# Optimization experiments

Hardware: AMD Instinct MI355X
Metric: run time of the kernel (lower is better)

The kernel has to match this reference:

```python
import jax, jax.numpy as jnp
import numpy as np

N_QUBITS = 8
N_LAYERS = 1
DIM = 1 << N_QUBITS  # 256 statevector amplitudes; PennyLane wire 0 = most significant bit

_idx = np.arange(DIM)
_BITS = np.stack([(_idx >> (N_QUBITS - 1 - w)) & 1 for w in range(N_QUBITS)])  # (n, D)
_FLIP = np.stack([_idx ^ (1 << (N_QUBITS - 1 - w)) for w in range(N_QUBITS)])  # (n, D)

def _cnot_perm(c, t):
    return _idx ^ (((_idx >> (N_QUBITS - 1 - c)) & 1) << (N_QUBITS - 1 - t))

_CNOT_NP = [_cnot_perm(w, w + 1) for w in range(N_QUBITS - 1)] + [_cnot_perm(N_QUBITS - 1, 0)]
BITS = jnp.asarray(_BITS)
FLIP = jnp.asarray(_FLIP)
CNOTS = [jnp.asarray(p) for p in _CNOT_NP]


def _ry(t):
    c = jnp.cos(t / 2)
    s = jnp.sin(t / 2)
    return jnp.stack([jnp.stack([c, -s], -1), jnp.stack([s, c], -1)], -2).astype(jnp.complex64)


def _rx(t):
    c = jnp.cos(t / 2).astype(jnp.complex64)
    s = (-1j) * jnp.sin(t / 2).astype(jnp.complex64)
    return jnp.stack([jnp.stack([c, s], -1), jnp.stack([s, c], -1)], -2)


def _rz(t):
    tc = t.astype(jnp.complex64)
    e0 = jnp.exp(-0.5j * tc)
    e1 = jnp.exp(0.5j * tc)
    z = jnp.zeros_like(e0)
    return jnp.stack([jnp.stack([e0, z], -1), jnp.stack([z, e1], -1)], -2)


def _apply(state, U, w):
    # state: (B, 2**n) complex64; U: (2,2) shared or (B,2,2) per-sample; wire w (MSB-first)
    B = state.shape[0]
    s = state.reshape(B, 1 << w, 2, -1)
    if U.ndim == 3:
        s = jnp.einsum('bij,bajc->baic', U, s)
    else:
        s = jnp.einsum('ij,bajc->baic', U, s)
    return s.reshape(B, DIM)


def _circuit(angles, weights):
    # angles: (B, n_qubits) float32; weights: (n_layers, n_qubits, 3) float32
    B = angles.shape[0]
    state = jnp.zeros((B, DIM), jnp.complex64).at[:, 0].set(1.0)
    for w in range(N_QUBITS):
        state = _apply(state, _ry(angles[:, w]), w)  # per-sample RY encoding
    for l in range(N_LAYERS):
        for w in range(N_QUBITS):
            state = _apply(state, _rx(weights[l, w, 0]), w)
            state = _apply(state, _ry(weights[l, w, 1]), w)
            state = _apply(state, _rz(weights[l, w, 2]), w)
        for p in CNOTS:  # CNOT ring entangler as basis permutation
            state = state[:, p]
    probs = jnp.abs(state) ** 2
    outs = []
    for w in range(N_QUBITS):
        overlap = jnp.conj(state) * state[:, FLIP[w]]
        sign = (1.0 - 2.0 * BITS[w]).astype(probs.dtype)
        outs.append(jnp.sum(jnp.real(overlap), -1))       # <X_w>
        outs.append(jnp.sum(sign * jnp.imag(overlap), -1))  # <Y_w>
        outs.append(jnp.sum(sign * probs, -1))            # <Z_w>
    return jnp.stack(outs, -1)  # (B, 3*n_qubits), order X0,Y0,Z0,X1,...


def setup_inputs() -> dict:
    key = jax.random.key(0)
    k1, k2, k3 = jax.random.split(key, 3)
    B, IN_DIM = 16384, 512
    h = jax.random.normal(k1, (B, IN_DIM), jnp.float32)
    W_pre = 0.02 * jax.random.normal(k2, (N_QUBITS, IN_DIM), jnp.float32)
    b_pre = jnp.zeros((N_QUBITS,), jnp.float32)
    weights = 0.01 * jax.random.normal(k3, (N_LAYERS, N_QUBITS, 3), jnp.float32)
    return {"h": h, "W_pre": W_pre, "b_pre": b_pre, "weights": weights}


def reference(h, W_pre, b_pre, weights):
    a = h @ W_pre.T + b_pre
    a = jnp.clip(jnp.tanh(a) * (jnp.pi / 2), -jnp.pi, jnp.pi)  # _scale_to_angles
    z = _circuit(a, weights)
    norm = jnp.linalg.norm(z, axis=-1, keepdims=True)
    return z / jnp.maximum(norm, 1e-12)  # F.normalize(dim=-1)
```

## Files before the change

kernel.cpp:

```cpp
#include <hip/hip_runtime.h>


__global__ __launch_bounds__(256) void vqc_fused(
    const float* __restrict__ h,
    const float* __restrict__ Wp,
    const float* __restrict__ bp,
    const float* __restrict__ wt,
    float* __restrict__ out,
    int B)
{
    const int lane = threadIdx.x & 63;
    const int wave = (blockIdx.x * blockDim.x + threadIdx.x) >> 6;

    const int row0 = wave * 2;
    if (row0 >= B) return;
    const int row1 = row0 + 1;

    const float4* W4 = (const float4*)Wp;
    float wf[8][8];
    #pragma unroll
    for (int q = 0; q < 8; ++q) {
        float4 w0 = W4[q * 128 + lane * 2 + 0];
        float4 w1 = W4[q * 128 + lane * 2 + 1];
        wf[q][0] = w0.x; wf[q][1] = w0.y; wf[q][2] = w0.z; wf[q][3] = w0.w;
        wf[q][4] = w1.x; wf[q][5] = w1.y; wf[q][6] = w1.z; wf[q][7] = w1.w;
    }

    const int b3 = (lane >> 3) & 1, b4 = (lane >> 4) & 1, b5 = (lane >> 5) & 1;
    const float4* H4 = (const float4*)h;

    float4 h00 = H4[row0 * 128 + lane * 2 + 0];
    float4 h01 = H4[row0 * 128 + lane * 2 + 1];
    float4 h10 = H4[(row1 < B ? row1 : row0) * 128 + lane * 2 + 0];
    float4 h11 = H4[(row1 < B ? row1 : row0) * 128 + lane * 2 + 1];

    float hf0[8] = { h00.x, h00.y, h00.z, h00.w, h01.x, h01.y, h01.z, h01.w };
    float hf1[8] = { h10.x, h10.y, h10.z, h10.w, h11.x, h11.y, h11.z, h11.w };

    float acc0[8], acc1[8];
    #pragma unroll
    for (int q = 0; q < 8; ++q) {
        float a0 = 0.f, a1 = 0.f;
        #pragma unroll
        for (int j = 0; j < 8; ++j) {
            a0 = fmaf(wf[q][j], hf0[j], a0);
            a1 = fmaf(wf[q][j], hf1[j], a1);
        }
        acc0[q] = a0; acc1[q] = a1;
    }

    float n0[4], n1[4];
    #pragma unroll
    for (int j = 0; j < 4; ++j) {
        float k0 = b3 ? acc0[1 + 2*j] : acc0[0 + 2*j];
        float s0 = b3 ? acc0[0 + 2*j] : acc0[1 + 2*j];
        float k1 = b3 ? acc1[1 + 2*j] : acc1[0 + 2*j];
        float s1 = b3 ? acc1[0 + 2*j] : acc1[1 + 2*j];
        n0[j] = k0 + __shfl_xor(s0, 8);
        n1[j] = k1 + __shfl_xor(s1, 8);
    }
    float m0[2], m1[2];
    #pragma unroll
    for (int i = 0; i < 2; ++i) {
        float k0 = b4 ? n0[1 + 2*i] : n0[0 + 2*i];
        float s0 = b4 ? n0[0 + 2*i] : n0[1 + 2*i];
        float k1 = b4 ? n1[1 + 2*i] : n1[0 + 2*i];
        float s1 = b4 ? n1[0 + 2*i] : n1[1 + 2*i];
        m0[i] = k0 + __shfl_xor(s0, 16);
        m1[i] = k1 + __shfl_xor(s1, 16);
    }
    float v0, v1;
    {
        float k0 = b5 ? m0[1] : m0[0];
        float s0 = b5 ? m0[0] : m0[1];
        float k1 = b5 ? m1[1] : m1[0];
        float s1 = b5 ? m1[0] : m1[1];
        v0 = k0 + __shfl_xor(s0, 32);
        v1 = k1 + __shfl_xor(s1, 32);
    }
    v0 += __shfl_xor(v0, 1); v1 += __shfl_xor(v1, 1);
    v0 += __shfl_xor(v0, 2); v1 += __shfl_xor(v1, 2);
    v0 += __shfl_xor(v0, 4); v1 += __shfl_xor(v1, 4);

    const int r = lane & 1;
    float vsel = r ? v1 : v0;
    float av[8];
    #pragma unroll
    for (int q = 0; q < 8; ++q) av[q] = __shfl(vsel, q * 8 + r);

    float X[8], Y[8], Z[8];
    #pragma unroll
    for (int q = 0; q < 8; ++q) {
        float t0 = wt[q * 3 + 0] * 0.5f;
        float t1 = wt[q * 3 + 1] * 0.5f;
        float t2 = wt[q * 3 + 2] * 0.5f;
        float s0, c0, s1, c1, sz, cz;
        __sincosf(t0, &s0, &c0);
        __sincosf(t1, &s1, &c1);
        __sincosf(t2, &sz, &cz);
        float N00r =  c1 * c0, N00i =  s1 * s0;
        float N01r = -s1 * c0, N01i = -c1 * s0;
        float N10r =  s1 * c0, N10i = -c1 * s0;
        float N11r =  c1 * c0, N11i = -s1 * s0;
        float M00r = cz * N00r + sz * N00i, M00i = cz * N00i - sz * N00r;
        float M01r = cz * N01r + sz * N01i, M01i = cz * N01i - sz * N01r;
        float M10r = cz * N10r - sz * N10i, M10i = cz * N10i + sz * N10r;
        float M11r = cz * N11r - sz * N11i, M11i = cz * N11i + sz * N11r;

        float a = av[q] + bp[q];
        a = fminf(fmaxf(a, -15.f), 15.f);
        float e = __expf(a + a);
        float th = (e - 1.f) / (e + 1.f);
        float phi = th * 0.78539816339744831f;
        float ss, cc;
        __sincosf(phi, &ss, &cc);
        float ar = M00r * cc + M01r * ss, ai = M00i * cc + M01i * ss;
        float br = M10r * cc + M11r * ss, bi = M10i * cc + M11i * ss;
        Z[q] = (ar * ar + ai * ai) - (br * br + bi * bi);
        X[q] = 2.f * (ar * br + ai * bi);
        Y[q] = 2.f * (ar * bi - ai * br);
    }

    float P[8], T[8];
    P[0] = Z[0];
    #pragma unroll
    for (int w = 1; w < 8; ++w) P[w] = P[w - 1] * Z[w];
    T[7] = Z[7];
    #pragma unroll
    for (int w = 6; w >= 0; --w) T[w] = Z[w] * T[w + 1];
    float Z2to6 = Z[2] * Z[3] * Z[4] * Z[5] * Z[6];

    float o[24];
    #pragma unroll
    for (int w = 0; w < 7; ++w) o[3 * w] = X[w] * X[w + 1];
    o[21] = X[7] * X[0] * X[1];
    o[1] = X[0] * Y[1] * T[2];
    #pragma unroll
    for (int w = 1; w < 7; ++w) o[3 * w + 1] = Y[w] * X[w + 1] * P[w - 1];
    o[22] = -Y[7] * Y[0] * Y[1] * Z2to6;
    o[2] = T[1];
    #pragma unroll
    for (int w = 1; w < 8; ++w) o[3 * w + 2] = P[w];

    float sq = 0.f;
    #pragma unroll
    for (int j = 0; j < 24; ++j) sq = fmaf(o[j], o[j], sq);
    float inv = 1.f / fmaxf(sqrtf(sq), 1e-12f);

    if (lane < 2) {
        const int row = row0 + lane;
        if (row < B) {
            float4* O4 = (float4*)(out + row * 24);
            #pragma unroll
            for (int j = 0; j < 6; ++j) {
                float4 vv = { o[4 * j] * inv, o[4 * j + 1] * inv,
                              o[4 * j + 2] * inv, o[4 * j + 3] * inv };
                O4[j] = vv;
            }
        }
    }
}

extern "C" void kernel_launch(void* const* d_in, const int* in_sizes, int n_in,
                              void* d_out, int out_size, void* d_ws, size_t ws_size,
                              hipStream_t stream) {
    const float* h  = (const float*)d_in[0];
    const float* Wp = (const float*)d_in[1];
    const float* bp = (const float*)d_in[2];
    const float* wt = (const float*)d_in[3];
    float* out = (float*)d_out;
    (void)d_ws; (void)ws_size;

    const int B = in_sizes[0] / 512;
    const int nblk = (B + 7) / 8;
    vqc_fused<<<nblk, 256, 0, stream>>>(h, Wp, bp, wt, out, B);
}
```

Baseline: 95.14 us.

## Process 64 rows per block with prefetched loads and LDS-staged per-row epilogue

Each block now handles 64 rows. Each wave loops over 16 rows two at a time and prefetches the next pair of h rows while reducing the current pair. The projected angles are written to shared memory, and one wave then runs the circuit epilogue with one thread per row. This replaces the old scheme where every wave redundantly ran the full epilogue for two rows on all 64 lanes. That redundancy is removed and the W loads are amortised over more rows, at the cost of fewer blocks (256), a barrier, and a serial epilogue in a single wave per block.

```diff
diff --git a/kernel.cpp b/kernel.cpp
--- a/kernel.cpp
+++ b/kernel.cpp
@@ -1,7 +1,7 @@
 #include <hip/hip_runtime.h>
 
 
-__global__ __launch_bounds__(256) void vqc_fused(
+__global__ __launch_bounds__(256, 1) void vqc_block64(
     const float* __restrict__ h,
     const float* __restrict__ Wp,
     const float* __restrict__ bp,
@@ -9,12 +9,14 @@
     float* __restrict__ out,
     int B)
 {
+    __shared__ float aw_lds[64][9];
+
     const int lane = threadIdx.x & 63;
-    const int wave = (blockIdx.x * blockDim.x + threadIdx.x) >> 6;
-
-    const int row0 = wave * 2;
-    if (row0 >= B) return;
-    const int row1 = row0 + 1;
+    const int wv   = threadIdx.x >> 6;
+    const int blockRow = blockIdx.x * 64;
+    const int waveRow  = blockRow + wv * 16;
+
+    const int b3 = (lane >> 3) & 1, b4 = (lane >> 4) & 1, b5 = (lane >> 5) & 1;
 
     const float4* W4 = (const float4*)Wp;
     float wf[8][8];
@@ -26,130 +28,155 @@
         wf[q][4] = w1.x; wf[q][5] = w1.y; wf[q][6] = w1.z; wf[q][7] = w1.w;
     }
 
-    const int b3 = (lane >> 3) & 1, b4 = (lane >> 4) & 1, b5 = (lane >> 5) & 1;
     const float4* H4 = (const float4*)h;
-
-    float4 h00 = H4[row0 * 128 + lane * 2 + 0];
-    float4 h01 = H4[row0 * 128 + lane * 2 + 1];
-    float4 h10 = H4[(row1 < B ? row1 : row0) * 128 + lane * 2 + 0];
-    float4 h11 = H4[(row1 < B ? row1 : row0) * 128 + lane * 2 + 1];
-
-    float hf0[8] = { h00.x, h00.y, h00.z, h00.w, h01.x, h01.y, h01.z, h01.w };
-    float hf1[8] = { h10.x, h10.y, h10.z, h10.w, h11.x, h11.y, h11.z, h11.w };
-
-    float acc0[8], acc1[8];
-    #pragma unroll
-    for (int q = 0; q < 8; ++q) {
-        float a0 = 0.f, a1 = 0.f;
+    const int Bm1 = B - 1;
+
+    if (waveRow < B) {
+        int r0 = waveRow < Bm1 ? waveRow : Bm1;
+        int r1 = waveRow + 1 < Bm1 ? waveRow + 1 : Bm1;
+        float4 p00 = H4[r0 * 128 + lane * 2 + 0];
+        float4 p01 = H4[r0 * 128 + lane * 2 + 1];
+        float4 p10 = H4[r1 * 128 + lane * 2 + 0];
+        float4 p11 = H4[r1 * 128 + lane * 2 + 1];
+
         #pragma unroll
-        for (int j = 0; j < 8; ++j) {
-            a0 = fmaf(wf[q][j], hf0[j], a0);
-            a1 = fmaf(wf[q][j], hf1[j], a1);
+        for (int p = 0; p < 8; ++p) {
+            float hf0[8] = { p00.x, p00.y, p00.z, p00.w,
+                             p01.x, p01.y, p01.z, p01.w };
+            float hf1[8] = { p10.x, p10.y, p10.z, p10.w,
+                             p11.x, p11.y, p11.z, p11.w };
+            if (p < 7) {
+                int n0 = waveRow + 2 * (p + 1);
+                int n1 = n0 + 1;
+                n0 = n0 < Bm1 ? n0 : Bm1;
+                n1 = n1 < Bm1 ? n1 : Bm1;
+                p00 = H4[n0 * 128 + lane * 2 + 0];
+                p01 = H4[n0 * 128 + lane * 2 + 1];
+                p10 = H4[n1 * 128 + lane * 2 + 0];
+                p11 = H4[n1 * 128 + lane * 2 + 1];
+            }
+
+            float acc0[8], acc1[8];
+            #pragma unroll
+            for (int q = 0; q < 8; ++q) {
+                float a0 = 0.f, a1 = 0.f;
+                #pragma unroll
+                for (int j = 0; j < 8; ++j) {
+                    a0 = fmaf(wf[q][j], hf0[j], a0);
+                    a1 = fmaf(wf[q][j], hf1[j], a1);
+                }
+                acc0[q] = a0; acc1[q] = a1;
+            }
+
+            float n0v[4], n1v[4];
+            #pragma unroll
+            for (int j = 0; j < 4; ++j) {
+                float k0 = b3 ? acc0[1 + 2*j] : acc0[0 + 2*j];
+                float s0 = b3 ? acc0[0 + 2*j] : acc0[1 + 2*j];
+                float k1 = b3 ? acc1[1 + 2*j] : acc1[0 + 2*j];
+                float s1 = b3 ? acc1[0 + 2*j] : acc1[1 + 2*j];
+                n0v[j] = k0 + __shfl_xor(s0, 8);
+                n1v[j] = k1 + __shfl_xor(s1, 8);
+            }
+            float m0v[2], m1v[2];
+            #pragma unroll
+            for (int i = 0; i < 2; ++i) {
+                float k0 = b4 ? n0v[1 + 2*i] : n0v[0 + 2*i];
+                float s0 = b4 ? n0v[0 + 2*i] : n0v[1 + 2*i];
+                float k1 = b4 ? n1v[1 + 2*i] : n1v[0 + 2*i];
+                float s1 = b4 ? n1v[0 + 2*i] : n1v[1 + 2*i];
+                m0v[i] = k0 + __shfl_xor(s0, 16);
+                m1v[i] = k1 + __shfl_xor(s1, 16);
+            }
+            float v0, v1;
+            {
+                float k0 = b5 ? m0v[1] : m0v[0];
+                float s0 = b5 ? m0v[0] : m0v[1];
+                float k1 = b5 ? m1v[1] : m1v[0];
+                float s1 = b5 ? m1v[0] : m1v[1];
+                v0 = k0 + __shfl_xor(s0, 32);
+                v1 = k1 + __shfl_xor(s1, 32);
+            }
+            v0 += __shfl_xor(v0, 1); v1 += __shfl_xor(v1, 1);
+            v0 += __shfl_xor(v0, 2); v1 += __shfl_xor(v1, 2);
+            v0 += __shfl_xor(v0, 4); v1 += __shfl_xor(v1, 4);
+
+            if ((lane & 7) == 0) {
+                int q = lane >> 3;
+                aw_lds[wv * 16 + 2 * p + 0][q] = v0;
+                aw_lds[wv * 16 + 2 * p + 1][q] = v1;
+            }
         }
-        acc0[q] = a0; acc1[q] = a1;
     }
 
-    float n0[4], n1[4];
-    #pragma unroll
-    for (int j = 0; j < 4; ++j) {
-        float k0 = b3 ? acc0[1 + 2*j] : acc0[0 + 2*j];
-        float s0 = b3 ? acc0[0 + 2*j] : acc0[1 + 2*j];
-        float k1 = b3 ? acc1[1 + 2*j] : acc1[0 + 2*j];
-        float s1 = b3 ? acc1[0 + 2*j] : acc1[1 + 2*j];
-        n0[j] = k0 + __shfl_xor(s0, 8);
-        n1[j] = k1 + __shfl_xor(s1, 8);
-    }
-    float m0[2], m1[2];
-    #pragma unroll
-    for (int i = 0; i < 2; ++i) {
-        float k0 = b4 ? n0[1 + 2*i] : n0[0 + 2*i];
-        float s0 = b4 ? n0[0 + 2*i] : n0[1 + 2*i];
-        float k1 = b4 ? n1[1 + 2*i] : n1[0 + 2*i];
-        float s1 = b4 ? n1[0 + 2*i] : n1[1 + 2*i];
-        m0[i] = k0 + __shfl_xor(s0, 16);
-        m1[i] = k1 + __shfl_xor(s1, 16);
-    }
-    float v0, v1;
-    {
-        float k0 = b5 ? m0[1] : m0[0];
-        float s0 = b5 ? m0[0] : m0[1];
-        float k1 = b5 ? m1[1] : m1[0];
-        float s1 = b5 ? m1[0] : m1[1];
-        v0 = k0 + __shfl_xor(s0, 32);
-        v1 = k1 + __shfl_xor(s1, 32);
-    }
-    v0 += __shfl_xor(v0, 1); v1 += __shfl_xor(v1, 1);
-    v0 += __shfl_xor(v0, 2); v1 += __shfl_xor(v1, 2);
-    v0 += __shfl_xor(v0, 4); v1 += __shfl_xor(v1, 4);
-
-    const int r = lane & 1;
-    float vsel = r ? v1 : v0;
-    float av[8];
-    #pragma unroll
-    for (int q = 0; q < 8; ++q) av[q] = __shfl(vsel, q * 8 + r);
-
-    float X[8], Y[8], Z[8];
-    #pragma unroll
-    for (int q = 0; q < 8; ++q) {
-        float t0 = wt[q * 3 + 0] * 0.5f;
-        float t1 = wt[q * 3 + 1] * 0.5f;
-        float t2 = wt[q * 3 + 2] * 0.5f;
-        float s0, c0, s1, c1, sz, cz;
-        __sincosf(t0, &s0, &c0);
-        __sincosf(t1, &s1, &c1);
-        __sincosf(t2, &sz, &cz);
-        float N00r =  c1 * c0, N00i =  s1 * s0;
-        float N01r = -s1 * c0, N01i = -c1 * s0;
-        float N10r =  s1 * c0, N10i = -c1 * s0;
-        float N11r =  c1 * c0, N11i = -s1 * s0;
-        float M00r = cz * N00r + sz * N00i, M00i = cz * N00i - sz * N00r;
-        float M01r = cz * N01r + sz * N01i, M01i = cz * N01i - sz * N01r;
-        float M10r = cz * N10r - sz * N10i, M10i = cz * N10i + sz * N10r;
-        float M11r = cz * N11r - sz * N11i, M11i = cz * N11i + sz * N11r;
-
-        float a = av[q] + bp[q];
-        a = fminf(fmaxf(a, -15.f), 15.f);
-        float e = __expf(a + a);
-        float th = (e - 1.f) / (e + 1.f);
-        float phi = th * 0.78539816339744831f;
-        float ss, cc;
-        __sincosf(phi, &ss, &cc);
-        float ar = M00r * cc + M01r * ss, ai = M00i * cc + M01i * ss;
-        float br = M10r * cc + M11r * ss, bi = M10i * cc + M11i * ss;
-        Z[q] = (ar * ar + ai * ai) - (br * br + bi * bi);
-        X[q] = 2.f * (ar * br + ai * bi);
-        Y[q] = 2.f * (ar * bi - ai * br);
-    }
-
-    float P[8], T[8];
-    P[0] = Z[0];
-    #pragma unroll
-    for (int w = 1; w < 8; ++w) P[w] = P[w - 1] * Z[w];
-    T[7] = Z[7];
-    #pragma unroll
-    for (int w = 6; w >= 0; --w) T[w] = Z[w] * T[w + 1];
-    float Z2to6 = Z[2] * Z[3] * Z[4] * Z[5] * Z[6];
-
-    float o[24];
-    #pragma unroll
-    for (int w = 0; w < 7; ++w) o[3 * w] = X[w] * X[w + 1];
-    o[21] = X[7] * X[0] * X[1];
-    o[1] = X[0] * Y[1] * T[2];
-    #pragma unroll
-    for (int w = 1; w < 7; ++w) o[3 * w + 1] = Y[w] * X[w + 1] * P[w - 1];
-    o[22] = -Y[7] * Y[0] * Y[1] * Z2to6;
-    o[2] = T[1];
-    #pragma unroll
-    for (int w = 1; w < 8; ++w) o[3 * w + 2] = P[w];
-
-    float sq = 0.f;
-    #pragma unroll
-    for (int j = 0; j < 24; ++j) sq = fmaf(o[j], o[j], sq);
-    float inv = 1.f / fmaxf(sqrtf(sq), 1e-12f);
-
-    if (lane < 2) {
-        const int row = row0 + lane;
+    __syncthreads();
+
+    if (threadIdx.x < 64) {
+        const int row = blockRow + (int)threadIdx.x;
         if (row < B) {
+            float av[8];
+            #pragma unroll
+            for (int q = 0; q < 8; ++q) av[q] = aw_lds[threadIdx.x][q];
+
+            float X[8], Y[8], Z[8];
+            #pragma unroll
+            for (int q = 0; q < 8; ++q) {
+                float t0 = wt[q * 3 + 0] * 0.5f;
+                float t1 = wt[q * 3 + 1] * 0.5f;
+                float t2 = wt[q * 3 + 2] * 0.5f;
+                float s0, c0, s1, c1, sz, cz;
+                __sincosf(t0, &s0, &c0);
+                __sincosf(t1, &s1, &c1);
+                __sincosf(t2, &sz, &cz);
+                float N00r =  c1 * c0, N00i =  s1 * s0;
+                float N01r = -s1 * c0, N01i = -c1 * s0;
+                float N10r =  s1 * c0, N10i = -c1 * s0;
+                float N11r =  c1 * c0, N11i = -s1 * s0;
+                float M00r = cz * N00r + sz * N00i, M00i = cz * N00i - sz * N00r;
+                float M01r = cz * N01r + sz * N01i, M01i = cz * N01i - sz * N01r;
+                float M10r = cz * N10r - sz * N10i, M10i = cz * N10i + sz * N10r;
+                float M11r = cz * N11r - sz * N11i, M11i = cz * N11i + sz * N11r;
+
+                float a = av[q] + bp[q];
+                a = fminf(fmaxf(a, -15.f), 15.f);
+                float e = __expf(a + a);
+                float th = (e - 1.f) / (e + 1.f);
+                float phi = th * 0.78539816339744831f;
+                float ss, cc;
+                __sincosf(phi, &ss, &cc);
+                float ar = M00r * cc + M01r * ss, ai = M00i * cc + M01i * ss;
+                float br = M10r * cc + M11r * ss, bi = M10i * cc + M11i * ss;
+                Z[q] = (ar * ar + ai * ai) - (br * br + bi * bi);
+                X[q] = 2.f * (ar * br + ai * bi);
+                Y[q] = 2.f * (ar * bi - ai * br);
+            }
+
+            float P[8], T[8];
+            P[0] = Z[0];
+            #pragma unroll
+            for (int w = 1; w < 8; ++w) P[w] = P[w - 1] * Z[w];
+            T[7] = Z[7];
+            #pragma unroll
+            for (int w = 6; w >= 0; --w) T[w] = Z[w] * T[w + 1];
+            float Z2to6 = Z[2] * Z[3] * Z[4] * Z[5] * Z[6];
+
+            float o[24];
+            #pragma unroll
+            for (int w = 0; w < 7; ++w) o[3 * w] = X[w] * X[w + 1];
+            o[21] = X[7] * X[0] * X[1];
+            o[1] = X[0] * Y[1] * T[2];
+            #pragma unroll
+            for (int w = 1; w < 7; ++w) o[3 * w + 1] = Y[w] * X[w + 1] * P[w - 1];
+            o[22] = -Y[7] * Y[0] * Y[1] * Z2to6;
+            o[2] = T[1];
+            #pragma unroll
+            for (int w = 1; w < 8; ++w) o[3 * w + 2] = P[w];
+
+            float sq = 0.f;
+            #pragma unroll
+            for (int j = 0; j < 24; ++j) sq = fmaf(o[j], o[j], sq);
+            float inv = 1.f / fmaxf(sqrtf(sq), 1e-12f);
+
             float4* O4 = (float4*)(out + row * 24);
             #pragma unroll
             for (int j = 0; j < 6; ++j) {
@@ -172,6 +199,6 @@
     (void)d_ws; (void)ws_size;
 
     const int B = in_sizes[0] / 512;
-    const int nblk = (B + 7) / 8;
-    vqc_fused<<<nblk, 256, 0, stream>>>(h, Wp, bp, wt, out, B);
+    const int nblk = (B + 63) / 64;
+    vqc_block64<<<nblk, 256, 0, stream>>>(h, Wp, bp, wt, out, B);
 }
```

Measured after the change: 80.95 us. 14.9% less time.
